# Optimization experiments

Hardware: AMD Instinct MI355X
Metric: run time of the kernel (lower is better)

## Reference

```python
import jax, jax.numpy as jnp
import numpy as np

LN_EPS = 1e-5
NEG_SLOPE = 0.01  # torch F.leaky_relu default


def setup_inputs() -> dict:
    key = jax.random.key(0)
    ks = jax.random.split(key, 12)
    B, N, Do, Na = 128, 32, 128, 16
    H, Dk, Dv = 4, 64, 64
    Dio = Do + Na  # 144
    g = lambda k, shape, fan_in: jax.random.normal(k, shape, jnp.float32) / np.sqrt(fan_in)
    return {
        "states": jax.random.normal(ks[0], (B, N, Do), jnp.float32),
        "policies": jax.random.uniform(ks[1], (B, N, Na), jnp.float32),
        "actions": jax.random.uniform(ks[2], (B, N, Na), jnp.float32),
        "W_se": g(ks[3], (Do, 128), Do),
        "b_se": jnp.zeros((128,), jnp.float32),
        "W_sape": g(ks[4], (Dio, 128), Dio),
        "b_sape": jnp.zeros((128,), jnp.float32),
        "Wk": g(ks[5], (H, 128, Dk), 128),
        "Wq": g(ks[6], (H, 128, Dk), 128),
        "Wv": g(ks[7], (H, 128, Dv), 128),
        "ln_g": jnp.ones((H, Dv), jnp.float32),
        "ln_b": jnp.zeros((H, Dv), jnp.float32),
        "W_f1": g(ks[8], (H * Dv, 64), H * Dv),
        "W_f2": g(ks[9], (64, 1), 64),
    }


def _layernorm(x, g, b):
    mu = x.mean(-1, keepdims=True)
    var = ((x - mu) ** 2).mean(-1, keepdims=True)
    return (x - mu) * jax.lax.rsqrt(var + LN_EPS) * g + b


def reference(states, policies, actions, W_se, b_se, W_sape, b_sape,
              Wk, Wq, Wv, ln_g, ln_b, W_f1, W_f2):
    leaky = lambda x: jax.nn.leaky_relu(x, NEG_SLOPE)
    B, N, _ = states.shape
    H, _, Dv = Wv.shape
    d_k = Wk.shape[-1]

    se = leaky(states @ W_se + b_se)  # [B,N,128]

    oa = jnp.concatenate([states, actions], axis=-1)   # [B,N,Dio]
    op = jnp.concatenate([states, policies], axis=-1)  # [B,N,Dio]
    # oap[b,j,k] = op[b,k] if j==k else oa[b,k]  (place_policies/place_actions masks)
    eye = jnp.eye(N, dtype=states.dtype)[None, :, :, None]  # [1,N,N,1]
    oap = eye * op[:, None, :, :] + (1.0 - eye) * oa[:, None, :, :]  # [B,N,N,Dio]
    x = leaky(oap @ W_sape + b_sape)  # [B,N,N,128]

    key = jnp.einsum('bnd,hde->bhne', se, Wk)  # [B,H,N,Dk]
    qry = jnp.einsum('bnd,hde->bhne', se, Wq)
    scores = jnp.einsum('bhie,bhke->bhik', qry, key) / jnp.sqrt(jnp.asarray(d_k, states.dtype))
    w = jax.nn.softmax(scores, axis=-1)  # [B,H,N,N]

    av = jnp.einsum('bjkd,hde->bhjke', x, Wv)  # [B,H,N,N,Dv]
    # node_features[b,h,i,j] = sum_k w[b,h,i,k] * av[b,h,j,k]  (fuses torch's O(N^3) repeat)
    nf = jnp.einsum('bhik,bhjke->bhije', w, av)  # [B,H,N,N,Dv]
    nf = _layernorm(nf, ln_g[None, :, None, None, :], ln_b[None, :, None, None, :])

    mh = jnp.moveaxis(nf, 1, 3).reshape(B, N, N, H * Dv)  # concat heads on last dim
    value = leaky(mh @ W_f1) @ W_f2  # [B,N,N,1]
    return value, w
```

## Files before the change

kernel.cpp:

```cpp
#include <hip/hip_runtime.h>
#include <hip/hip_bf16.h>

#define B 128
#define N 32
#define DO 128
#define NA 16
#define H 4
#define DK 64
#define DV 64
#define LN_EPS 1e-5f
#define NEG_SLOPE 0.01f

typedef unsigned short u16;
typedef __attribute__((ext_vector_type(8))) short bf16x8;
typedef __attribute__((ext_vector_type(4))) float f32x4;

__device__ __forceinline__ float leaky(float x) {
    return x >= 0.f ? x : NEG_SLOPE * x;
}

__device__ __forceinline__ u16 f2bf(float x) {
    union { float f; unsigned int u; } v; v.f = x;
    unsigned int r = (v.u + 0x7FFF + ((v.u >> 16) & 1)) >> 16;
    return (u16)r;
}

__device__ __forceinline__ float bf2f(u16 x) {
    union { unsigned int u; float f; } v; v.u = ((unsigned int)x) << 16;
    return v.f;
}

template<int CTRL>
__device__ __forceinline__ float dppadd(float x) {
    return x + __int_as_float(__builtin_amdgcn_update_dpp(
        0, __float_as_int(x), CTRL, 0xF, 0xF, true));
}

__global__ __launch_bounds__(256) void kP(
    const float* __restrict__ Wk, const float* __restrict__ Wq,
    const float* __restrict__ Wv, const float* __restrict__ W_se,
    const float* __restrict__ W_sape, const float* __restrict__ ln_g,
    const float* __restrict__ ln_b, const float* __restrict__ W_f1,
    u16* __restrict__ wTb, u16* __restrict__ wseT, u16* __restrict__ wsapeT,
    u16* __restrict__ sapeTail, u16* __restrict__ wTg,
    float* __restrict__ GW, float* __restrict__ BW)
{
    const int blk = blockIdx.x;
    const int t   = threadIdx.x;
    __shared__ float wls[8192];

    if (blk < 4) {
        const int hh = blk;
        for (int m = 0; m < 3; m++) {
            const float* src = (m == 0 ? Wq : (m == 1 ? Wk : Wv)) + hh * 8192;
            for (int idx = t; idx < 2048; idx += 256)
                ((float4*)wls)[idx] = ((const float4*)src)[idx];
            __syncthreads();
            u16* dst = wTb + (hh * 3 + m) * 8192;
            for (int idx = t; idx < 8192; idx += 256) {
                const int n = idx >> 7, k = idx & 127;
                dst[idx] = f2bf(wls[k * 64 + n]);
            }
            __syncthreads();
        }
    } else if (blk == 4 || blk == 5) {
        const float* src = (blk == 4) ? W_se : W_sape;
        u16* dst = (blk == 4) ? wseT : wsapeT;
        for (int chunk = 0; chunk < 2; chunk++) {
            const int k0 = chunk * 64;
            for (int idx = t; idx < 2048; idx += 256)
                ((float4*)wls)[idx] = ((const float4*)(src + k0 * 128))[idx];
            __syncthreads();
            for (int idx = t; idx < 8192; idx += 256) {
                const int n = idx >> 6, kk = idx & 63;
                dst[n * 128 + k0 + kk] = f2bf(wls[kk * 128 + n]);
            }
            __syncthreads();
        }
        if (blk == 5) {
            for (int idx = t; idx < 2048; idx += 256)
                wls[idx] = W_sape[128 * 128 + idx];
            __syncthreads();
            for (int idx = t; idx < 4096; idx += 256) {
                const int n = idx >> 5, kk = idx & 31;
                sapeTail[n * 32 + kk] = (kk < 16) ? f2bf(wls[kk * 128 + n]) : (u16)0;
            }
        }
    } else {
        for (int idx = t; idx < 16384; idx += 256) {
            const int hh = idx >> 12, c = (idx >> 6) & 63, ee = idx & 63;
            wTg[idx] = f2bf(ln_g[hh * 64 + ee] * W_f1[(hh * 64 + ee) * 64 + c]);
        }
        {
            const int hh = t >> 6, c = t & 63;
            float g = 0.f;
            #pragma unroll 4
            for (int ee = 0; ee < 64; ee++)
                g += ln_g[hh * 64 + ee] * W_f1[(hh * 64 + ee) * 64 + c];
            GW[t] = g;
        }
        {
            const int c = t & 63, qq = t >> 6;
            float bacc = 0.f;
            #pragma unroll 4
            for (int r = 0; r < 64; r++)
                bacc += ln_b[qq * 64 + r] * W_f1[(qq * 64 + r) * 64 + c];
            wls[qq * 64 + c] = bacc;
        }
        __syncthreads();
        if (t < 64) BW[t] = wls[t] + wls[64 + t] + wls[128 + t] + wls[192 + t];
    }
}

__global__ __launch_bounds__(1024, 8) void kB(
    const float* __restrict__ states, const float* __restrict__ actions,
    const float* __restrict__ policies,
    const float* __restrict__ b_se, const float* __restrict__ b_sape,
    const u16* __restrict__ wTb, const u16* __restrict__ wseT,
    const u16* __restrict__ wsapeT, const u16* __restrict__ sapeTail,
    const u16* __restrict__ wTg,
    float* __restrict__ w_out,
    float* __restrict__ SG, float* __restrict__ DG,
    float* __restrict__ sumS, float* __restrict__ sumS2,
    float* __restrict__ sumD, float* __restrict__ sumD2,
    float* __restrict__ dotSD)
{
    const int bh   = blockIdx.x;
    const int b    = bh >> 2;
    const int h    = bh & 3;
    const int t    = threadIdx.x;
    const int wave = t >> 6;
    const int e    = t & 63;
    const int q16  = e >> 4;
    const int l16  = e & 15;

    __shared__ alignas(16) u16   sST[32 * 136];
    __shared__ alignas(16) u16   actA[32 * 40];
    __shared__ alignas(16) u16   polA[32 * 40];
    __shared__ alignas(16) u16   sSE[32 * 136];
    __shared__ alignas(16) u16   sXA[32 * 136];
    __shared__ alignas(16) u16   sXP[32 * 136];
    __shared__ alignas(16) u16   qb[32 * 72];
    __shared__ alignas(16) u16   kb[32 * 72];
    __shared__ alignas(16) u16   avaT[64 * 40];
    __shared__ alignas(16) u16   diffb[32 * 72];
    __shared__ alignas(16) u16   wb[32 * 40];
    __shared__ alignas(16) float S32[32 * 68];
    __shared__ alignas(16) u16   Sb[32 * 72];

    {
        const int r = t >> 5, c4 = (t & 31) * 4;
        const float4 s4 = *(const float4*)&states[(b * 32 + r) * 128 + c4];
        ushort4 u;
        u.x = f2bf(s4.x); u.y = f2bf(s4.y); u.z = f2bf(s4.z); u.w = f2bf(s4.w);
        *(ushort4*)&sST[r * 136 + c4] = u;
    }
    if (t < 512) {
        const int r = t >> 4, c = t & 15;
        actA[r * 40 + c]      = f2bf(actions[(b * 32 + r) * 16 + c]);
        actA[r * 40 + 16 + c] = 0;
    } else {
        const int t2 = t - 512, r = t2 >> 4, c = t2 & 15;
        polA[r * 40 + c]      = f2bf(policies[(b * 32 + r) * 16 + c]);
        polA[r * 40 + 16 + c] = 0;
    }
    __syncthreads();

    {
        const int mt = wave >> 3, nt = wave & 7;
        const int arow = mt * 16 + l16;
        const int bcol = nt * 16 + l16;
        f32x4 a_se = {0.f,0.f,0.f,0.f}, a_sp = {0.f,0.f,0.f,0.f};
        f32x4 a_oa = {0.f,0.f,0.f,0.f}, a_op = {0.f,0.f,0.f,0.f};
        const u16* bse_p = wseT + bcol * 128;
        const u16* bsp_p = wsapeT + bcol * 128;
        #pragma unroll
        for (int ks = 0; ks < 4; ks++) {
            const bf16x8 af = *(const bf16x8*)&sST[arow * 136 + ks * 32 + q16 * 8];
            a_se = __builtin_amdgcn_mfma_f32_16x16x32_bf16(
                af, *(const bf16x8*)&bse_p[ks * 32 + q16 * 8], a_se, 0, 0, 0);
            a_sp = __builtin_amdgcn_mfma_f32_16x16x32_bf16(
                af, *(const bf16x8*)&bsp_p[ks * 32 + q16 * 8], a_sp, 0, 0, 0);
        }
        const bf16x8 bt = *(const bf16x8*)&sapeTail[bcol * 32 + q16 * 8];
        a_oa = __builtin_amdgcn_mfma_f32_16x16x32_bf16(
            *(const bf16x8*)&actA[arow * 40 + q16 * 8], bt, a_oa, 0, 0, 0);
        a_op = __builtin_amdgcn_mfma_f32_16x16x32_bf16(
            *(const bf16x8*)&polA[arow * 40 + q16 * 8], bt, a_op, 0, 0, 0);
        const float bse_c = b_se[bcol];
        const float bsp_c = b_sape[bcol];
        const int r0 = mt * 16 + q16 * 4;
        #pragma unroll
        for (int v = 0; v < 4; v++) {
            sSE[(r0 + v) * 136 + bcol] = f2bf(leaky(a_se[v] + bse_c));
            sXA[(r0 + v) * 136 + bcol] = f2bf(leaky(a_sp[v] + a_oa[v] + bsp_c));
            sXP[(r0 + v) * 136 + bcol] = f2bf(leaky(a_sp[v] + a_op[v] + bsp_c));
        }
    }
    __syncthreads();

    f32x4 acc[2];
    #pragma unroll
    for (int p = 0; p < 2; p++) {
        const int tau = wave * 2 + p;
        const int mat = tau >> 3;
        const int mt  = (tau >> 2) & 1, nt = tau & 3;
        const u16* X  = (mat <= 1) ? sSE : (mat == 2 ? sXA : sXP);
        const int widx = (mat == 0) ? 0 : (mat == 1 ? 1 : 2);
        const int arow = mt * 16 + l16;
        const u16* wsrc = wTb + ((h * 3 + widx) * 64 + nt * 16 + l16) * 128;
        f32x4 a = {0.f, 0.f, 0.f, 0.f};
        #pragma unroll
        for (int ks = 0; ks < 4; ks++) {
            const bf16x8 af = *(const bf16x8*)&X[arow * 136 + ks * 32 + q16 * 8];
            const bf16x8 bf = *(const bf16x8*)&wsrc[ks * 32 + q16 * 8];
            a = __builtin_amdgcn_mfma_f32_16x16x32_bf16(af, bf, a, 0, 0, 0);
        }
        acc[p] = a;
    }
    #pragma unroll
    for (int p = 0; p < 2; p++) {
        const int tau = wave * 2 + p;
        const int mat = tau >> 3;
        const int mt  = (tau >> 2) & 1, nt = tau & 3;
        const int c   = nt * 16 + l16;
        const int r0  = mt * 16 + q16 * 4;
        if (mat == 0) {
            #pragma unroll
            for (int v = 0; v < 4; v++) qb[(r0 + v) * 72 + c] = f2bf(acc[p][v]);
        } else if (mat == 1) {
            #pragma unroll
            for (int v = 0; v < 4; v++) kb[(r0 + v) * 72 + c] = f2bf(acc[p][v]);
        } else if (mat == 2) {
            #pragma unroll
            for (int v = 0; v < 4; v++) avaT[c * 40 + (r0 + v)] = f2bf(acc[p][v]);
        }
    }
    __syncthreads();

    if (wave < 2) {
        const int mt = wave;
        f32x4 s0 = {0.f,0.f,0.f,0.f}, s1 = {0.f,0.f,0.f,0.f};
        #pragma unroll
        for (int ks = 0; ks < 2; ks++) {
            const bf16x8 af = *(const bf16x8*)&qb[(mt * 16 + l16) * 72 + ks * 32 + q16 * 8];
            const bf16x8 b0 = *(const bf16x8*)&kb[l16 * 72 + ks * 32 + q16 * 8];
            const bf16x8 b1 = *(const bf16x8*)&kb[(16 + l16) * 72 + ks * 32 + q16 * 8];
            s0 = __builtin_amdgcn_mfma_f32_16x16x32_bf16(af, b0, s0, 0, 0, 0);
            s1 = __builtin_amdgcn_mfma_f32_16x16x32_bf16(af, b1, s1, 0, 0, 0);
        }
        #pragma unroll
        for (int v = 0; v < 4; v++) {
            float a0 = s0[v] * 0.125f, a1 = s1[v] * 0.125f;
            float mx = fmaxf(a0, a1);
            #pragma unroll
            for (int m = 1; m < 16; m <<= 1) mx = fmaxf(mx, __shfl_xor(mx, m));
            float e0 = __expf(a0 - mx), e1 = __expf(a1 - mx);
            float sm = e0 + e1;
            #pragma unroll
            for (int m = 1; m < 16; m <<= 1) sm += __shfl_xor(sm, m);
            const float inv = 1.f / sm;
            e0 *= inv; e1 *= inv;
            const int i = mt * 16 + q16 * 4 + v;
            wb[i * 40 + l16]      = f2bf(e0);
            wb[i * 40 + 16 + l16] = f2bf(e1);
            w_out[(bh * 32 + i) * 32 + l16]      = e0;
            w_out[(bh * 32 + i) * 32 + 16 + l16] = e1;
        }
    } else if (wave >= 12) {
        #pragma unroll
        for (int p = 0; p < 2; p++) {
            const int tau = wave * 2 + p;
            const int mt  = (tau >> 2) & 1, nt = tau & 3;
            const int c   = nt * 16 + l16;
            const int r0  = mt * 16 + q16 * 4;
            #pragma unroll
            for (int v = 0; v < 4; v++) {
                const float av = bf2f(avaT[c * 40 + (r0 + v)]);
                diffb[(r0 + v) * 72 + c] = f2bf(acc[p][v] - av);
            }
        }
    }
    __syncthreads();

    if (wave < 8) {
        const int mt = wave >> 2, nt = wave & 3;
        const bf16x8 af = *(const bf16x8*)&wb[(mt * 16 + l16) * 40 + q16 * 8];
        const bf16x8 bf = *(const bf16x8*)&avaT[(nt * 16 + l16) * 40 + q16 * 8];
        f32x4 a = {0.f, 0.f, 0.f, 0.f};
        a = __builtin_amdgcn_mfma_f32_16x16x32_bf16(af, bf, a, 0, 0, 0);
        const int c = nt * 16 + l16, r0 = mt * 16 + q16 * 4;
        #pragma unroll
        for (int v = 0; v < 4; v++) {
            S32[(r0 + v) * 68 + c] = a[v];
            Sb[(r0 + v) * 72 + c]  = f2bf(a[v]);
        }
    } else {
        const int w8 = wave - 8;
        const int mt = w8 >> 2, nt = w8 & 3;
        const u16* wgp = wTg + (h * 64 + nt * 16 + l16) * 64;
        f32x4 a = {0.f, 0.f, 0.f, 0.f};
        #pragma unroll
        for (int ks = 0; ks < 2; ks++) {
            const bf16x8 af = *(const bf16x8*)&diffb[(mt * 16 + l16) * 72 + ks * 32 + q16 * 8];
            const bf16x8 bf = *(const bf16x8*)&wgp[ks * 32 + q16 * 8];
            a = __builtin_amdgcn_mfma_f32_16x16x32_bf16(af, bf, a, 0, 0, 0);
        }
        const int c = nt * 16 + l16, r0 = mt * 16 + q16 * 4;
        #pragma unroll
        for (int v = 0; v < 4; v++)
            DG[(bh * 32 + r0 + v) * 64 + c] = a[v];
    }
    if (t < 32) {
        float s1 = 0.f, s2 = 0.f;
        #pragma unroll
        for (int e8 = 0; e8 < 8; e8++) {
            const uint4 u = *(const uint4*)&diffb[t * 72 + e8 * 8];
            const unsigned int uu[4] = {u.x, u.y, u.z, u.w};
            #pragma unroll
            for (int q = 0; q < 4; q++) {
                const float fl = __uint_as_float(uu[q] << 16);
                const float fh = __uint_as_float(uu[q] & 0xffff0000u);
                s1 += fl + fh;
                s2 += fl * fl + fh * fh;
            }
        }
        sumD[bh * 32 + t] = s1; sumD2[bh * 32 + t] = s2;
    }
    __syncthreads();

    if (wave < 4) {
        const int mt = wave >> 1, nt = wave & 1;
        f32x4 a = {0.f, 0.f, 0.f, 0.f};
        #pragma unroll
        for (int ks = 0; ks < 2; ks++) {
            const bf16x8 af = *(const bf16x8*)&Sb[(mt * 16 + l16) * 72 + ks * 32 + q16 * 8];
            const bf16x8 bf = *(const bf16x8*)&diffb[(nt * 16 + l16) * 72 + ks * 32 + q16 * 8];
            a = __builtin_amdgcn_mfma_f32_16x16x32_bf16(af, bf, a, 0, 0, 0);
        }
        const int j = nt * 16 + l16, r0 = mt * 16 + q16 * 4;
        #pragma unroll
        for (int v = 0; v < 4; v++)
            dotSD[(bh * 32 + r0 + v) * 32 + j] = a[v];
    } else if (wave >= 8) {
        const int w8 = wave - 8;
        const int mt = w8 >> 2, nt = w8 & 3;
        const u16* wgp = wTg + (h * 64 + nt * 16 + l16) * 64;
        f32x4 a = {0.f, 0.f, 0.f, 0.f};
        #pragma unroll
        for (int ks = 0; ks < 2; ks++) {
            const bf16x8 af = *(const bf16x8*)&Sb[(mt * 16 + l16) * 72 + ks * 32 + q16 * 8];
            const bf16x8 bf = *(const bf16x8*)&wgp[ks * 32 + q16 * 8];
            a = __builtin_amdgcn_mfma_f32_16x16x32_bf16(af, bf, a, 0, 0, 0);
        }
        const int c = nt * 16 + l16, r0 = mt * 16 + q16 * 4;
        #pragma unroll
        for (int v = 0; v < 4; v++)
            SG[(bh * 32 + r0 + v) * 64 + c] = a[v];
    } else if (t >= 256 && t < 288) {
        const int r = t - 256;
        float s1 = 0.f, s2 = 0.f;
        #pragma unroll
        for (int e4 = 0; e4 < 16; e4++) {
            const float4 v4 = *(const float4*)&S32[r * 68 + e4 * 4];
            s1 += v4.x + v4.y + v4.z + v4.w;
            s2 += v4.x * v4.x + v4.y * v4.y + v4.z * v4.z + v4.w * v4.w;
        }
        sumS[bh * 32 + r] = s1; sumS2[bh * 32 + r] = s2;
    }
}

__global__ __launch_bounds__(256) void kC(
    const float* __restrict__ SG, const float* __restrict__ DG,
    const float* __restrict__ sumS, const float* __restrict__ sumS2,
    const float* __restrict__ sumD, const float* __restrict__ sumD2,
    const float* __restrict__ dotSD, const float* __restrict__ w_all,
    const float* __restrict__ GW, const float* __restrict__ BW,
    const float* __restrict__ W_f2, float* __restrict__ value)
{
    const int blk = blockIdx.x;
    const int b   = blk >> 3;
    const int i0  = ((blk >> 1) & 3) * 8;
    const int j0  = (blk & 1) * 16;
    const int t   = threadIdx.x;
    const int w0  = t >> 6;
    const int e   = t & 63;

    __shared__ alignas(16) float pk[8 * 16 * 12];

    for (int idx = t; idx < 512; idx += 256) {
        const int ii = idx >> 6, jl = (idx >> 2) & 15, hh = idx & 3;
        const int j  = j0 + jl;
        const int hi = (b * 4 + hh) * 32 + i0 + ii;
        const int hj = (b * 4 + hh) * 32 + j;
        const float wv  = w_all[hi * 32 + j];
        const float dsd = dotSD[hi * 32 + j];
        const float mu  = (sumS[hi] + wv * sumD[hj]) * (1.f / 64.f);
        const float e2  = (sumS2[hi] + 2.f * wv * dsd + wv * wv * sumD2[hj]) * (1.f / 64.f);
        const float var = fmaxf(e2 - mu * mu, 0.f);
        const float inv = rsqrtf(var + LN_EPS);
        float* rec = &pk[(ii * 16 + jl) * 12 + hh * 3];
        rec[0] = inv;
        rec[1] = inv * wv;
        rec[2] = -inv * mu;
    }

    const float bwr = BW[e];
    const float f2v = W_f2[e];
    float gw[4], sg[8][4];
    #pragma unroll
    for (int hh = 0; hh < 4; hh++) {
        gw[hh] = GW[hh * 64 + e];
        #pragma unroll
        for (int ii = 0; ii < 8; ii++)
            sg[ii][hh] = SG[((b * 4 + hh) * 32 + i0 + ii) * 64 + e];
    }
    __syncthreads();

    for (int jb = 0; jb < 4; jb++) {
        const int jl = jb * 4 + w0;
        const int j  = j0 + jl;
        float d[4];
        #pragma unroll
        for (int hh = 0; hh < 4; hh++)
            d[hh] = DG[((b * 4 + hh) * 32 + j) * 64 + e];
        #pragma unroll
        for (int ii = 0; ii < 8; ii++) {
            const float* rec = &pk[(ii * 16 + jl) * 12];
            const f32x4 r0 = *(const f32x4*)rec;
            const f32x4 r1 = *(const f32x4*)(rec + 4);
            const f32x4 r2 = *(const f32x4*)(rec + 8);
            float z = bwr;
            z += r0[0] * sg[ii][0]; z += r0[1] * d[0]; z += r0[2] * gw[0];
            z += r0[3] * sg[ii][1]; z += r1[0] * d[1]; z += r1[1] * gw[1];
            z += r1[2] * sg[ii][2]; z += r1[3] * d[2]; z += r2[0] * gw[2];
            z += r2[1] * sg[ii][3]; z += r2[2] * d[3]; z += r2[3] * gw[3];
            float p = leaky(z) * f2v;
            p = dppadd<0x111>(p);
            p = dppadd<0x112>(p);
            p = dppadd<0x114>(p);
            p = dppadd<0x118>(p);
            p = dppadd<0x142>(p);
            p = dppadd<0x143>(p);
            if (e == 63) value[(b * 32 + i0 + ii) * 32 + j] = p;
        }
    }
}

extern "C" void kernel_launch(void* const* d_in, const int* in_sizes, int n_in,
                              void* d_out, int out_size, void* d_ws, size_t ws_size,
                              hipStream_t stream)
{
    const float* states   = (const float*)d_in[0];
    const float* policies = (const float*)d_in[1];
    const float* actions  = (const float*)d_in[2];
    const float* W_se     = (const float*)d_in[3];
    const float* b_se     = (const float*)d_in[4];
    const float* W_sape   = (const float*)d_in[5];
    const float* b_sape   = (const float*)d_in[6];
    const float* Wk       = (const float*)d_in[7];
    const float* Wq       = (const float*)d_in[8];
    const float* Wv       = (const float*)d_in[9];
    const float* ln_g     = (const float*)d_in[10];
    const float* ln_b     = (const float*)d_in[11];
    const float* W_f1     = (const float*)d_in[12];
    const float* W_f2     = (const float*)d_in[13];

    float* out_value = (float*)d_out;
    float* out_w     = out_value + B * N * N;

    float* ws    = (float*)d_ws;
    float* SG    = ws;
    float* DG    = SG    + 1048576;
    float* sumS  = DG    + 1048576;
    float* sumS2 = sumS  + 16384;
    float* sumD  = sumS2 + 16384;
    float* sumD2 = sumD  + 16384;
    float* dotSD = sumD2 + 16384;
    float* GW    = dotSD + 524288;
    float* BW    = GW    + 256;
    u16*   wTb   = (u16*)(BW + 64);
    u16*   wseT  = wTb   + 98304;
    u16*   wsapeT= wseT  + 16384;
    u16*   sapeTail = wsapeT + 16384;
    u16*   wTg   = sapeTail + 4096;

    kP<<<7, 256, 0, stream>>>(Wk, Wq, Wv, W_se, W_sape, ln_g, ln_b, W_f1,
                              wTb, wseT, wsapeT, sapeTail, wTg, GW, BW);
    kB<<<B * H, 1024, 0, stream>>>(states, actions, policies, b_se, b_sape,
                                   wTb, wseT, wsapeT, sapeTail, wTg, out_w,
                                   SG, DG, sumS, sumS2, sumD, sumD2, dotSD);
    kC<<<B * 8, 256, 0, stream>>>(SG, DG, sumS, sumS2, sumD, sumD2, dotSD,
                                  out_w, GW, BW, W_f2, out_value);
}
```

Before: 133.9 us.

## Fuse final MLP stage into attention kernel via per-batch atomic barrier

Removes the separate kC launch and instead has the four head-blocks of each batch sync through a global atomic counter, then compute the value MLP directly. LayerNorm statistics records are computed per lane and broadcast with readlane instead of going through shared memory. This saves a launch and the gap between kernels. The cost is a spin-wait that relies on all four blocks of a batch being co-resident, so it risks deadlock or stalls when they are not.

```diff
diff --git a/kernel.cpp b/kernel.cpp
--- a/kernel.cpp
+++ b/kernel.cpp
@@ -36,6 +36,10 @@
         0, __float_as_int(x), CTRL, 0xF, 0xF, true));
 }
 
+__device__ __forceinline__ float rdlane(float x, int lane) {
+    return __int_as_float(__builtin_amdgcn_readlane(__float_as_int(x), lane));
+}
+
 __global__ __launch_bounds__(256) void kP(
     const float* __restrict__ Wk, const float* __restrict__ Wq,
     const float* __restrict__ Wv, const float* __restrict__ W_se,
@@ -43,7 +47,8 @@
     const float* __restrict__ ln_b, const float* __restrict__ W_f1,
     u16* __restrict__ wTb, u16* __restrict__ wseT, u16* __restrict__ wsapeT,
     u16* __restrict__ sapeTail, u16* __restrict__ wTg,
-    float* __restrict__ GW, float* __restrict__ BW)
+    float* __restrict__ GW, float* __restrict__ BW,
+    unsigned int* __restrict__ cnt)
 {
     const int blk = blockIdx.x;
     const int t   = threadIdx.x;
@@ -87,6 +92,7 @@
             }
         }
     } else {
+        if (t < 128) cnt[t] = 0u;
         for (int idx = t; idx < 16384; idx += 256) {
             const int hh = idx >> 12, c = (idx >> 6) & 63, ee = idx & 63;
             wTg[idx] = f2bf(ln_g[hh * 64 + ee] * W_f1[(hh * 64 + ee) * 64 + c]);
@@ -123,7 +129,10 @@
     float* __restrict__ SG, float* __restrict__ DG,
     float* __restrict__ sumS, float* __restrict__ sumS2,
     float* __restrict__ sumD, float* __restrict__ sumD2,
-    float* __restrict__ dotSD)
+    float* __restrict__ dotSD,
+    const float* __restrict__ GW, const float* __restrict__ BW,
+    const float* __restrict__ W_f2, float* __restrict__ value,
+    unsigned int* __restrict__ cnt)
 {
     const int bh   = blockIdx.x;
     const int b    = bh >> 2;
@@ -368,81 +377,83 @@
         }
         sumS[bh * 32 + r] = s1; sumS2[bh * 32 + r] = s2;
     }
-}
-
-__global__ __launch_bounds__(256) void kC(
-    const float* __restrict__ SG, const float* __restrict__ DG,
-    const float* __restrict__ sumS, const float* __restrict__ sumS2,
-    const float* __restrict__ sumD, const float* __restrict__ sumD2,
-    const float* __restrict__ dotSD, const float* __restrict__ w_all,
-    const float* __restrict__ GW, const float* __restrict__ BW,
-    const float* __restrict__ W_f2, float* __restrict__ value)
-{
-    const int blk = blockIdx.x;
-    const int b   = blk >> 3;
-    const int i0  = ((blk >> 1) & 3) * 8;
-    const int j0  = (blk & 1) * 16;
-    const int t   = threadIdx.x;
-    const int w0  = t >> 6;
-    const int e   = t & 63;
-
-    __shared__ alignas(16) float pk[8 * 16 * 12];
-
-    for (int idx = t; idx < 512; idx += 256) {
-        const int ii = idx >> 6, jl = (idx >> 2) & 15, hh = idx & 3;
-        const int j  = j0 + jl;
-        const int hi = (b * 4 + hh) * 32 + i0 + ii;
-        const int hj = (b * 4 + hh) * 32 + j;
-        const float wv  = w_all[hi * 32 + j];
-        const float dsd = dotSD[hi * 32 + j];
-        const float mu  = (sumS[hi] + wv * sumD[hj]) * (1.f / 64.f);
-        const float e2  = (sumS2[hi] + 2.f * wv * dsd + wv * wv * sumD2[hj]) * (1.f / 64.f);
-        const float var = fmaxf(e2 - mu * mu, 0.f);
-        const float inv = rsqrtf(var + LN_EPS);
-        float* rec = &pk[(ii * 16 + jl) * 12 + hh * 3];
-        rec[0] = inv;
-        rec[1] = inv * wv;
-        rec[2] = -inv * mu;
-    }
-
-    const float bwr = BW[e];
-    const float f2v = W_f2[e];
-    float gw[4], sg[8][4];
-    #pragma unroll
-    for (int hh = 0; hh < 4; hh++) {
-        gw[hh] = GW[hh * 64 + e];
-        #pragma unroll
-        for (int ii = 0; ii < 8; ii++)
-            sg[ii][hh] = SG[((b * 4 + hh) * 32 + i0 + ii) * 64 + e];
-    }
-    __syncthreads();
-
-    for (int jb = 0; jb < 4; jb++) {
-        const int jl = jb * 4 + w0;
-        const int j  = j0 + jl;
-        float d[4];
-        #pragma unroll
-        for (int hh = 0; hh < 4; hh++)
-            d[hh] = DG[((b * 4 + hh) * 32 + j) * 64 + e];
-        #pragma unroll
-        for (int ii = 0; ii < 8; ii++) {
-            const float* rec = &pk[(ii * 16 + jl) * 12];
-            const f32x4 r0 = *(const f32x4*)rec;
-            const f32x4 r1 = *(const f32x4*)(rec + 4);
-            const f32x4 r2 = *(const f32x4*)(rec + 8);
-            float z = bwr;
-            z += r0[0] * sg[ii][0]; z += r0[1] * d[0]; z += r0[2] * gw[0];
-            z += r0[3] * sg[ii][1]; z += r1[0] * d[1]; z += r1[1] * gw[1];
-            z += r1[2] * sg[ii][2]; z += r1[3] * d[2]; z += r2[0] * gw[2];
-            z += r2[1] * sg[ii][3]; z += r2[2] * d[3]; z += r2[3] * gw[3];
-            float p = leaky(z) * f2v;
-            p = dppadd<0x111>(p);
-            p = dppadd<0x112>(p);
-            p = dppadd<0x114>(p);
-            p = dppadd<0x118>(p);
-            p = dppadd<0x142>(p);
-            p = dppadd<0x143>(p);
-            if (e == 63) value[(b * 32 + i0 + ii) * 32 + j] = p;
+
+    __threadfence();
+    __syncthreads();
+    if (t == 0) {
+        __hip_atomic_fetch_add(&cnt[b], 1u, __ATOMIC_RELEASE, __HIP_MEMORY_SCOPE_AGENT);
+        while (__hip_atomic_load(&cnt[b], __ATOMIC_ACQUIRE, __HIP_MEMORY_SCOPE_AGENT) < 4u) {}
+    }
+    __syncthreads();
+
+    {
+        const int i0   = h * 8;
+        const int jg   = wave >> 3;
+        const int wsub = wave & 7;
+        const int j_0  = jg * 16 + wsub * 2;
+
+        const float bwr = BW[e];
+        const float f2v = W_f2[e];
+        float gw[4];
+        #pragma unroll
+        for (int hh = 0; hh < 4; hh++) gw[hh] = GW[hh * 64 + e];
+
+        const int rii  = (e & 31) >> 2;
+        const int rhh  = e & 3;
+        const int hi_r = (b * 4 + rhh) * 32 + i0 + rii;
+
+        float ra[2], rb2[2], rc[2];
+        #pragma unroll
+        for (int jb = 0; jb < 2; jb++) {
+            const int j    = j_0 + jb;
+            const int hj_r = (b * 4 + rhh) * 32 + j;
+            const float wv  = w_out[hi_r * 32 + j];
+            const float dsd = dotSD[hi_r * 32 + j];
+            const float mu  = (sumS[hi_r] + wv * sumD[hj_r]) * (1.f / 64.f);
+            const float e2  = (sumS2[hi_r] + 2.f * wv * dsd + wv * wv * sumD2[hj_r]) * (1.f / 64.f);
+            const float var = fmaxf(e2 - mu * mu, 0.f);
+            const float inv = rsqrtf(var + LN_EPS);
+            ra[jb]  = inv;
+            rb2[jb] = inv * wv;
+            rc[jb]  = -inv * mu;
+        }
+
+        float z[2][8];
+        #pragma unroll
+        for (int jb = 0; jb < 2; jb++)
+            #pragma unroll
+            for (int ii = 0; ii < 8; ii++) z[jb][ii] = bwr;
+
+        #pragma unroll
+        for (int hh = 0; hh < 4; hh++) {
+            const float d0 = DG[((b * 4 + hh) * 32 + j_0    ) * 64 + e];
+            const float d1 = DG[((b * 4 + hh) * 32 + j_0 + 1) * 64 + e];
+            #pragma unroll
+            for (int ii = 0; ii < 8; ii++) {
+                const float sgv = SG[((b * 4 + hh) * 32 + i0 + ii) * 64 + e];
+                const int lane = ii * 4 + hh;
+                z[0][ii] += rdlane(ra[0],  lane) * sgv;
+                z[0][ii] += rdlane(rb2[0], lane) * d0;
+                z[0][ii] += rdlane(rc[0],  lane) * gw[hh];
+                z[1][ii] += rdlane(ra[1],  lane) * sgv;
+                z[1][ii] += rdlane(rb2[1], lane) * d1;
+                z[1][ii] += rdlane(rc[1],  lane) * gw[hh];
+            }
+        }
+
+        #pragma unroll
+        for (int jb = 0; jb < 2; jb++) {
+            #pragma unroll
+            for (int ii = 0; ii < 8; ii++) {
+                float p = leaky(z[jb][ii]) * f2v;
+                p = dppadd<0x111>(p);
+                p = dppadd<0x112>(p);
+                p = dppadd<0x114>(p);
+                p = dppadd<0x118>(p);
+                p = dppadd<0x142>(p);
+                p = dppadd<0x143>(p);
+                if (e == 63) value[(b * 32 + i0 + ii) * 32 + (j_0 + jb)] = p;
+            }
         }
     }
 }
@@ -484,12 +495,12 @@
     u16*   wsapeT= wseT  + 16384;
     u16*   sapeTail = wsapeT + 16384;
     u16*   wTg   = sapeTail + 4096;
+    unsigned int* cnt = (unsigned int*)(wTg + 16384);
 
     kP<<<7, 256, 0, stream>>>(Wk, Wq, Wv, W_se, W_sape, ln_g, ln_b, W_f1,
-                              wTb, wseT, wsapeT, sapeTail, wTg, GW, BW);
+                              wTb, wseT, wsapeT, sapeTail, wTg, GW, BW, cnt);
     kB<<<B * H, 1024, 0, stream>>>(states, actions, policies, b_se, b_sape,
                                    wTb, wseT, wsapeT, sapeTail, wTg, out_w,
-                                   SG, DG, sumS, sumS2, sumD, sumD2, dotSD);
-    kC<<<B * 8, 256, 0, stream>>>(SG, DG, sumS, sumS2, sumD, sumD2, dotSD,
-                                  out_w, GW, BW, W_f2, out_value);
-}
+                                   SG, DG, sumS, sumS2, sumD, sumD2, dotSD,
+                                   GW, BW, W_f2, out_value, cnt);
+}
```

Result: slower. 335.4 us (+150.4%).
